# Kernel tuning notes

Measured on AMD Instinct MI355X. Metric: run time of the kernel, lower is better.

Reference implementation:

```python
import jax, jax.numpy as jnp
import numpy as np

T = 8        # n_segment
T_OUT = 8    # t_out
G = 4        # n_group
K = 3        # correlation_neighbor


def setup_inputs() -> dict:
    key = jax.random.key(0)
    k1, k2, k3 = jax.random.split(key, 3)
    x = jax.random.normal(k1, (64, 256, 56, 56), dtype=jnp.float32)
    # grouped 1x1 conv: in=G*(T-1)*K*K=252 (63 per group), out=T_OUT*G*T=256 (64 per group)
    conv_w = jax.random.normal(k2, (G, T_OUT * T, (T - 1) * K * K), dtype=jnp.float32) * 0.05
    conv_b = jax.random.normal(k3, (G, T_OUT * T), dtype=jnp.float32) * 0.05
    return {"x": x, "conv_w": conv_w, "conv_b": conv_b}


def reference(x, conv_w, conv_b):
    nt, c, h, w = x.shape
    nb = nt // T
    cpg = c // G
    pad = K // 2

    x5 = x.reshape(nb, T, c, h, w)
    # ReplicationPad2d(pad) on spatial dims
    xp = jnp.pad(x5, ((0, 0), (0, 0), (0, 0), (pad, pad), (pad, pad)), mode='edge')

    # 9-way shifted cost volume: per-group channel-sum of x[t] * x_pad[t+1] shifted
    a = x5[:, :T - 1].reshape(nb, T - 1, G, cpg, h, w)
    corr_list = []
    for i in range(K):
        for j in range(K):
            b = xp[:, 1:, :, i:i + h, j:j + w].reshape(nb, T - 1, G, cpg, h, w)
            corr_list.append(jnp.einsum('ntgchw,ntgchw->ntghw', a, b))
    corr = jnp.stack(corr_list, axis=3)                     # (nb, T-1, G, K*K, h, w)
    corr = corr.transpose(0, 2, 1, 3, 4, 5)                 # (nb, G, T-1, K*K, h, w)
    corr = corr.reshape(nb, G, (T - 1) * K * K, h, w)

    # grouped 1x1 conv
    wx = jnp.einsum('ngihw,goi->ngohw', corr, conv_w) + conv_b[None, :, :, None, None]
    wx = wx.reshape(nb, G, T_OUT, T, h, w).transpose(2, 1, 0, 3, 4, 5)  # (t_out, G, nb, T, h, w)

    # torch splits c as (c_per_group, G) here (c_per_group outer) — mimic exactly
    xs = x5.reshape(nb, T, cpg, G, h, w).transpose(2, 3, 0, 1, 4, 5)   # (cpg, G, nb, T, h, w)

    # weighted segment-sum over T for each output frame
    xsum = jnp.einsum('ognthw,cgnthw->ocgnhw', wx, xs)      # (t_out, cpg, G, nb, h, w)

    # residual: x at frame floor(i*T/t_out)
    i_in = (np.arange(T_OUT) * T) // T_OUT
    res = xs[:, :, :, i_in].transpose(3, 0, 1, 2, 4, 5)     # (t_out, cpg, G, nb, h, w)

    out = (xsum + res).transpose(3, 0, 2, 1, 4, 5)          # (nb, t_out, G, cpg, h, w)
    return out.reshape(nb * T_OUT, c, h, w)
```

## Files before the change

kernel.cpp:

```cpp
#include <hip/hip_runtime.h>

namespace {
constexpr int NBb = 8;
constexpr int TT  = 8;
constexpr int TOo = 8;
constexpr int CC  = 256;
constexpr int GG  = 4;
constexpr int CPG = 64;
constexpr int HHH = 56;
constexpr int WWW = 56;
constexpr int HWs = HHH * WWW;
constexpr long CHW = (long)CC * HWs;
constexpr int NC  = (TT - 1) * 9;
constexpr long CORR_ELEMS = (long)NBb * GG * NC * HWs;
}

__global__ __launch_bounds__(64, 8)
void corr_k(const float* __restrict__ x, float* __restrict__ corr)
{
    const int lid = blockIdx.x + 392 * (blockIdx.y + 4 * blockIdx.z);
    const int wg  = (lid & 7) * 1568 + (lid >> 3);
    const int bx  = wg % 392;
    const int rem = wg / 392;
    const int g   = rem & 3;
    const int n   = rem >> 2;
    const int t   = bx / HHH;
    const int h   = bx % HHH;

    const int w  = threadIdx.x;
    const int wc = w < WWW - 1 ? w : WWW - 1;
    const int hm = h > 0 ? h - 1 : 0;
    const int hp = h < HHH - 1 ? h + 1 : HHH - 1;

    const float* xa = x + (long)n * TT * CHW + (long)g * CPG * HWs + (long)t * CHW;
    const float* xb = xa + CHW;
    const int offh = h  * WWW + wc;
    const int offm = hm * WWW + wc;
    const int offp = hp * WWW + wc;

    float acc[9];
#pragma unroll
    for (int k = 0; k < 9; ++k) acc[k] = 0.0f;

#pragma unroll 4
    for (int c = 0; c < CPG; ++c) {
        const long co = (long)c * HWs;
        const float a  = xa[co + offh];
        const float bm = xb[co + offm];
        const float bc = xb[co + offh];
        const float bp = xb[co + offp];
        float bml = __shfl_up(bm, 1), bmr = __shfl_down(bm, 1);
        float bcl = __shfl_up(bc, 1), bcr = __shfl_down(bc, 1);
        float bpl = __shfl_up(bp, 1), bpr = __shfl_down(bp, 1);
        if (w == 0) { bml = bm; bcl = bc; bpl = bp; }
        acc[0] = fmaf(a, bml, acc[0]); acc[1] = fmaf(a, bm, acc[1]); acc[2] = fmaf(a, bmr, acc[2]);
        acc[3] = fmaf(a, bcl, acc[3]); acc[4] = fmaf(a, bc, acc[4]); acc[5] = fmaf(a, bcr, acc[5]);
        acc[6] = fmaf(a, bpl, acc[6]); acc[7] = fmaf(a, bp, acc[7]); acc[8] = fmaf(a, bpr, acc[8]);
    }

    if (w < WWW) {
        float* co = corr + ((((long)n * GG + g) * 7 + t) * 9) * HWs + h * WWW + w;
#pragma unroll
        for (int k = 0; k < 9; ++k) co[(long)k * HWs] = acc[k];
    }
}

__global__ __launch_bounds__(256, 2)
void fuse_k(const float* __restrict__ x, const float* __restrict__ corr,
            const float* __restrict__ conv_w, const float* __restrict__ conv_b,
            float* __restrict__ out)
{
    __shared__ float swx[64][64];

    const int tid  = threadIdx.x;
    const int w    = tid & 63;
    const int wave = tid >> 6;
    const int wc   = w < WWW - 1 ? w : WWW - 1;
    const int h = blockIdx.x;
    const int g = blockIdx.y;
    const int n = blockIdx.z;

    float cr[NC];
    const float* cbase = corr + (((long)n * GG + g) * NC) * HWs + h * WWW;
#pragma unroll
    for (int i = 0; i < NC; ++i) cr[i] = cbase[(long)i * HWs + wc];

    const float* cw = conv_w + (long)g * (TOo * TT) * NC;
    const float* cb = conv_b + g * (TOo * TT);
#pragma unroll
    for (int oo = 0; oo < 16; ++oo) {
        const int o = wave * 16 + oo;
        float s = cb[o];
#pragma unroll
        for (int i = 0; i < NC; ++i) s = fmaf(cw[o * NC + i], cr[i], s);
        swx[o][w] = s;
    }
    __syncthreads();

    float wxr[TOo * TT];
#pragma unroll
    for (int o = 0; o < TOo * TT; ++o) wxr[o] = swx[o][w];

    const float* xn = x   + (long)n * TT  * CHW;
    float*       on = out + (long)n * TOo * CHW;
    for (int cpi = 0; cpi < 16; ++cpi) {
        const int cp = wave * 16 + cpi;
        const float* xc = xn + (long)(cp * GG + g) * HWs + h * WWW + wc;
        float xv[TT];
#pragma unroll
        for (int t = 0; t < TT; ++t) xv[t] = xc[(long)t * CHW];
        if (w < WWW) {
            float* oc = on + (long)(g * CPG + cp) * HWs + h * WWW + w;
#pragma unroll
            for (int to = 0; to < TOo; ++to) {
                float s = xv[to];
#pragma unroll
                for (int t = 0; t < TT; ++t) s = fmaf(wxr[to * TT + t], xv[t], s);
                oc[(long)to * CHW] = s;
            }
        }
    }
}

__global__ __launch_bounds__(64, 2)
void corr_fusion_mono(const float* __restrict__ x,
                      const float* __restrict__ conv_w,
                      const float* __restrict__ conv_b,
                      float* __restrict__ out)
{
    const int w  = threadIdx.x;
    const int wc = w < WWW - 1 ? w : WWW - 1;
    const int h  = blockIdx.x;
    const int g  = blockIdx.y;
    const int n  = blockIdx.z;
    const int hm = h > 0 ? h - 1 : 0;
    const int hp = h < HHH - 1 ? h + 1 : HHH - 1;

    const int offh = h  * WWW + wc;
    const int offm = hm * WWW + wc;
    const int offp = hp * WWW + wc;

    float corr[NC];
#pragma unroll
    for (int i = 0; i < NC; ++i) corr[i] = 0.0f;

    const float* xg = x + (long)n * TT * CHW + (long)g * CPG * HWs;

    for (int c = 0; c < CPG; ++c) {
        const float* xc = xg + (long)c * HWs;
        float rh[TT], rm[TT - 1], rp[TT - 1];
#pragma unroll
        for (int t = 0; t < TT; ++t) rh[t] = xc[(long)t * CHW + offh];
#pragma unroll
        for (int t = 1; t < TT; ++t) {
            rm[t - 1] = xc[(long)t * CHW + offm];
            rp[t - 1] = xc[(long)t * CHW + offp];
        }
#pragma unroll
        for (int t = 0; t < TT - 1; ++t) {
            const float a = rh[t];
#pragma unroll
            for (int di = 0; di < 3; ++di) {
                float bc = (di == 0) ? rm[t] : (di == 1) ? rh[t + 1] : rp[t];
                float bl = __shfl_up(bc, 1);
                if (w == 0) bl = bc;
                float br = __shfl_down(bc, 1);
                if (w == WWW - 1) br = bc;
                const int base = t * 9 + di * 3;
                corr[base + 0] = fmaf(a, bl, corr[base + 0]);
                corr[base + 1] = fmaf(a, bc, corr[base + 1]);
                corr[base + 2] = fmaf(a, br, corr[base + 2]);
            }
        }
    }

    const float* cw = conv_w + (long)g * (TOo * TT) * NC;
    const float* cb = conv_b + g * (TOo * TT);
    float wx[TOo * TT];
#pragma unroll
    for (int o = 0; o < TOo * TT; ++o) {
        float s = cb[o];
#pragma unroll
        for (int i = 0; i < NC; ++i) s = fmaf(cw[o * NC + i], corr[i], s);
        wx[o] = s;
    }

    const float* xn = x   + (long)n * TT  * CHW;
    float*       on = out + (long)n * TOo * CHW;
    for (int cp = 0; cp < CPG; ++cp) {
        const float* xc = xn + (long)(cp * GG + g) * HWs + offh;
        float xv[TT];
#pragma unroll
        for (int t = 0; t < TT; ++t) xv[t] = xc[(long)t * CHW];
        if (w < WWW) {
            float* oc = on + (long)(g * CPG + cp) * HWs + h * WWW + w;
#pragma unroll
            for (int to = 0; to < TOo; ++to) {
                float s = xv[to];
#pragma unroll
                for (int t = 0; t < TT; ++t) s = fmaf(wx[to * TT + t], xv[t], s);
                oc[(long)to * CHW] = s;
            }
        }
    }
}

extern "C" void kernel_launch(void* const* d_in, const int* in_sizes, int n_in,
                              void* d_out, int out_size, void* d_ws, size_t ws_size,
                              hipStream_t stream) {
    const float* x  = (const float*)d_in[0];
    const float* cw = (const float*)d_in[1];
    const float* cb = (const float*)d_in[2];
    float* out = (float*)d_out;

    if (ws_size >= CORR_ELEMS * sizeof(float)) {
        float* corr = (float*)d_ws;
        dim3 gridA(7 * HHH, GG, NBb);
        hipLaunchKernelGGL(corr_k, gridA, dim3(64), 0, stream, x, corr);
        dim3 gridB(HHH, GG, NBb);
        hipLaunchKernelGGL(fuse_k, gridB, dim3(256), 0, stream, x, corr, cw, cb, out);
    } else {
        dim3 grid(HHH, GG, NBb);
        hipLaunchKernelGGL(corr_fusion_mono, grid, dim3(64), 0, stream, x, cw, cb, out);
    }
}
```

Baseline: 516.7 us.

## Split fused conv+segment-sum into separate conv and segment kernels via workspace

Replaces the single fuse_k stage with two kernels: conv_k computes the grouped 1x1 conv weights into a new workspace buffer, and seg_k reads those weights and computes the weighted segment sum over smaller channel chunks. The aim is more, smaller blocks for higher occupancy and parallelism, since fuse_k has only 1792 blocks, uses large register arrays and does serial channel loops. In exchange it writes and re-reads an extra wx tensor of about 51 MB and adds a kernel launch, and this path runs only if the workspace is large enough.

```diff
diff --git a/kernel.cpp b/kernel.cpp
--- a/kernel.cpp
+++ b/kernel.cpp
@@ -13,6 +13,7 @@
 constexpr long CHW = (long)CC * HWs;
 constexpr int NC  = (TT - 1) * 9;
 constexpr long CORR_ELEMS = (long)NBb * GG * NC * HWs;
+constexpr long WX_ELEMS   = (long)NBb * GG * (TOo * TT) * HWs;
 }
 
 __global__ __launch_bounds__(64, 8)
@@ -65,6 +66,78 @@
     }
 }
 
+__global__ __launch_bounds__(64, 4)
+void conv_k(const float* __restrict__ corr,
+            const float* __restrict__ conv_w, const float* __restrict__ conv_b,
+            float* __restrict__ wxws)
+{
+    const int w   = threadIdx.x;
+    const int wc  = w < WWW - 1 ? w : WWW - 1;
+    const int h   = blockIdx.x;
+    const int by  = blockIdx.y;
+    const int g   = by >> 2;
+    const int och = by & 3;
+    const int n   = blockIdx.z;
+
+    const float* cbase = corr + (((long)n * GG + g) * NC) * HWs + h * WWW + wc;
+    float cr[NC];
+#pragma unroll
+    for (int i = 0; i < NC; ++i) cr[i] = cbase[(long)i * HWs];
+
+    const float* cw = conv_w + (long)g * (TOo * TT) * NC;
+    const float* cb = conv_b + g * (TOo * TT);
+    float* wbase = wxws + (((long)n * GG + g) * (TOo * TT)) * HWs + h * WWW + w;
+
+#pragma unroll
+    for (int oo = 0; oo < 16; ++oo) {
+        const int o = och * 16 + oo;
+        float s = cb[o];
+#pragma unroll
+        for (int i = 0; i < NC; ++i) s = fmaf(cw[o * NC + i], cr[i], s);
+        if (w < WWW) wbase[(long)o * HWs] = s;
+    }
+}
+
+__global__ __launch_bounds__(64, 4)
+void seg_k(const float* __restrict__ x, const float* __restrict__ wxws,
+           float* __restrict__ out)
+{
+    const int w   = threadIdx.x;
+    const int wc  = w < WWW - 1 ? w : WWW - 1;
+    const int h   = blockIdx.x;
+    const int by  = blockIdx.y;
+    const int g   = by >> 3;
+    const int cch = by & 7;
+    const int n   = blockIdx.z;
+
+    const float* wbase = wxws + (((long)n * GG + g) * (TOo * TT)) * HWs + h * WWW + wc;
+    float wxr[TOo * TT];
+#pragma unroll
+    for (int o = 0; o < TOo * TT; ++o) wxr[o] = wbase[(long)o * HWs];
+
+    const float* xn = x   + (long)n * TT  * CHW;
+    float*       on = out + (long)n * TOo * CHW;
+
+#pragma unroll
+    for (int cpi = 0; cpi < 8; ++cpi) {
+        const int cp = cch * 8 + cpi;
+        const float* xc = xn + (long)(cp * GG + g) * HWs + h * WWW + wc;
+        float xv[TT];
+#pragma unroll
+        for (int t = 0; t < TT; ++t) xv[t] = xc[(long)t * CHW];
+        if (w < WWW) {
+            float* oc = on + (long)(g * CPG + cp) * HWs + h * WWW + w;
+#pragma unroll
+            for (int to = 0; to < TOo; ++to) {
+                float s = xv[to];
+#pragma unroll
+                for (int t = 0; t < TT; ++t) s = fmaf(wxr[to * TT + t], xv[t], s);
+                oc[(long)to * CHW] = s;
+            }
+        }
+    }
+}
+
 __global__ __launch_bounds__(256, 2)
 void fuse_k(const float* __restrict__ x, const float* __restrict__ corr,
             const float* __restrict__ conv_w, const float* __restrict__ conv_b,
@@ -213,7 +286,16 @@
     const float* cb = (const float*)d_in[2];
     float* out = (float*)d_out;
 
-    if (ws_size >= CORR_ELEMS * sizeof(float)) {
+    if (ws_size >= (CORR_ELEMS + WX_ELEMS) * sizeof(float)) {
+        float* corr = (float*)d_ws;
+        float* wxws = corr + CORR_ELEMS;
+        dim3 gridA(7 * HHH, GG, NBb);
+        hipLaunchKernelGGL(corr_k, gridA, dim3(64), 0, stream, x, corr);
+        dim3 gridC(HHH, GG * 4, NBb);
+        hipLaunchKernelGGL(conv_k, gridC, dim3(64), 0, stream, corr, cw, cb, wxws);
+        dim3 gridS(HHH, GG * 8, NBb);
+        hipLaunchKernelGGL(seg_k, gridS, dim3(64), 0, stream, x, wxws, out);
+    } else if (ws_size >= CORR_ELEMS * sizeof(float)) {
         float* corr = (float*)d_ws;
         dim3 gridA(7 * HHH, GG, NBb);
         hipLaunchKernelGGL(corr_k, gridA, dim3(64), 0, stream, x, corr);
```

Result: faster. 492.3 us (-4.7%).
